# Performance work log

Hardware: AMD Instinct MI355X
Metric: run time of the kernel (lower is better)

Reference implementation:

```python
import jax, jax.numpy as jnp
import numpy as np

# --- model dims (from init args) ---
LAYERS = 6
LEAF = 2 ** (LAYERS - 1)        # 32
M_LEN = 128
CAM_NUM = 2
MAIN_CAM = 0
LATENT = 48
H_LAT = 2048                    # LatentNet hidden
H_BR = 512                      # ChooseBranchNet hidden
B = 16384

# Path bits: for leaf i, bit at classifier depth d (root->leaf order) is
# (i >> (LAYERS-2-d)) & 1. This is exactly what the search_table + double
# advanced-indexing gather in the torch code computes (heap tree routing).
_BITS = ((np.arange(LEAF)[:, None] >> np.arange(LAYERS - 2, -1, -1)[None, :]) & 1)  # [LEAF, LAYERS-1]
BITS = jnp.asarray(_BITS, dtype=jnp.int32)


def setup_inputs() -> dict:
    key = jax.random.key(0)
    ks = jax.random.split(key, 9)
    s = lambda fan: 1.0 / np.sqrt(fan)
    return {
        "batch_data": jax.random.normal(ks[0], (B, CAM_NUM, M_LEN), dtype=jnp.float32),
        # LatentNet: [B, 2*M_LEN] -> hidden -> LEAF*LATENT
        "Wl1": jax.random.normal(ks[1], (2 * M_LEN, H_LAT), dtype=jnp.float32) * s(2 * M_LEN),
        "bl1": jnp.zeros((H_LAT,), dtype=jnp.float32),
        "Wl2": jax.random.normal(ks[2], (H_LAT, LEAF * LATENT), dtype=jnp.float32) * s(H_LAT),
        "bl2": jnp.zeros((LEAF * LATENT,), dtype=jnp.float32),
        # ChooseBranchNet (shared across the LAYERS-1 classifier slots): M_LEN -> hidden -> 2
        "Wb1": jax.random.normal(ks[3], (M_LEN, H_BR), dtype=jnp.float32) * s(M_LEN),
        "bb1": jnp.zeros((H_BR,), dtype=jnp.float32),
        "Wb2": jax.random.normal(ks[4], (H_BR, 2), dtype=jnp.float32) * s(H_BR),
        "bb2": jnp.zeros((2,), dtype=jnp.float32),
    }


def reference(batch_data, Wl1, bl1, Wl2, bl2, Wb1, bb1, Wb2, bb2):
    bsz = batch_data.shape[0]
    # expand_measurements: main cam repeated (LAYERS-1) times -> [B, LAYERS-1, M_LEN]
    main = batch_data[:, MAIN_CAM]                                  # [B, M_LEN]
    x_br = jnp.broadcast_to(main[:, None, :], (bsz, LAYERS - 1, M_LEN))
    # ChooseBranchNet -> per-layer 2-way probabilities
    h = jax.nn.relu(jnp.einsum('blm,mh->blh', x_br, Wb1) + bb1)
    p = jax.nn.softmax(jnp.einsum('blh,ho->blo', h, Wb2) + bb2, axis=-1)  # [B, L-1, 2]
    # Tree gates: product of path-branch probabilities along root->leaf path.
    comp = jnp.where(BITS[None] == 1, p[:, None, :, 1], p[:, None, :, 0])  # [B, LEAF, L-1]
    gates = jnp.prod(comp, axis=-1)                                        # [B, LEAF]
    # top-1 routing (argsort(...)[:, -1] as in the torch code)
    router = jnp.argsort(gates, axis=-1)[:, -1]                            # [B]
    # LatentNet on concatenated two-camera measurements
    x2 = jnp.concatenate([batch_data[:, 0], batch_data[:, 1]], axis=-1)    # [B, 2*M_LEN]
    hl = jax.nn.relu(x2 @ Wl1 + bl1)
    nn_latent = (hl @ Wl2 + bl2).reshape(bsz, LEAF, LATENT)
    # scatter-select per-sample leaf latent (replaces the torch.where loop)
    select = jnp.take_along_axis(nn_latent, router[:, None, None], axis=1)[:, 0]  # [B, LATENT]
    return select
```

## Files before the change

### kernel.cpp

```cpp
#include <hip/hip_runtime.h>
#include <stdint.h>

typedef short bf16x8 __attribute__((ext_vector_type(8)));
typedef float f32x4 __attribute__((ext_vector_type(4)));

#define NROWS 16384
#define K1DIM 256
#define N1DIM 2048
#define N2DIM 96
#define MARGIN 0.03f

#define GLD16(g, l) __builtin_amdgcn_global_load_lds( \
    (const __attribute__((address_space(1))) uint32_t*)(g), \
    (__attribute__((address_space(3))) uint32_t*)(l), 16, 0, 0)

__device__ __forceinline__ ushort f2bf(float x) {
  union { float f; uint32_t u; } c; c.f = x;
  uint32_t u = c.u;
  return (ushort)((u + 0x7FFFu + ((u >> 16) & 1u)) >> 16);
}

__global__ __launch_bounds__(256) void k0_convert(
    const float* __restrict__ bd, const float* __restrict__ Wl1,
    const float* __restrict__ Wl2, const float* __restrict__ Wb1,
    ushort* __restrict__ x2bf, ushort* __restrict__ wl1t,
    ushort* __restrict__ w2t, ushort* __restrict__ wb1t) {
  int i = blockIdx.x * 256 + threadIdx.x;
  {
    float4 v = ((const float4*)bd)[i];
    ushort4 o;
    o.x = f2bf(v.x); o.y = f2bf(v.y); o.z = f2bf(v.z); o.w = f2bf(v.w);
    ((ushort4*)x2bf)[i] = o;
  }
  if (i < 2048 * 256) {
    int n = i >> 8, k = i & 255;
    wl1t[i] = f2bf(Wl1[k * 2048 + n]);
  }
  if (i < 96 * 2048) {
    int j = i >> 11, k = i & 2047;
    int col = (j < 48) ? j : (1440 + j);
    w2t[i] = f2bf(Wl2[k * 1536 + col]);
  }
  if (i < 512 * 128) {
    int j = i >> 7, m = i & 127;
    wb1t[i] = f2bf(Wb1[m * 512 + j]);
  }
}

__global__ __launch_bounds__(256) void k1a_score(
    const ushort* __restrict__ x2bf, const ushort* __restrict__ wb1t,
    const float* __restrict__ bb1, const float* __restrict__ Wb2,
    float* __restrict__ part) {
  __shared__ __align__(1024) ushort As[128 * 64];
  __shared__ __align__(1024) ushort Bs[128 * 64];
  const int t = threadIdx.x, ln = t & 63, wv = t >> 6;
  const int m0 = blockIdx.y << 7;
  const int n0 = blockIdx.x << 7;
  const int wm = (wv >> 1) << 6, wn = (wv & 1) << 6;
  const int rsub = ln >> 3, kc8 = ln & 7;
  const int q = ln >> 4, rr = ln & 15;

  f32x4 acc[4][4] = {};

  for (int k0 = 0; k0 < 128; k0 += 64) {
#pragma unroll
    for (int i = 0; i < 4; i++) {
      int inst = (wv << 2) + i;
      int row = (inst << 3) + rsub;
      GLD16(x2bf + (size_t)(m0 + row) * 256 + k0 + (kc8 << 3), As + (inst << 9));
      GLD16(wb1t + (size_t)(n0 + row) * 128 + k0 + (kc8 << 3), Bs + (inst << 9));
    }
    __syncthreads();
#pragma unroll
    for (int kk = 0; kk < 2; kk++) {
      int kb = ((kk << 2) + q) << 3;
      bf16x8 af[4], bfr[4];
#pragma unroll
      for (int mi = 0; mi < 4; mi++)
        af[mi] = *(const bf16x8*)(As + (((wm + (mi << 4) + rr)) << 6) + kb);
#pragma unroll
      for (int ni = 0; ni < 4; ni++)
        bfr[ni] = *(const bf16x8*)(Bs + (((wn + (ni << 4) + rr)) << 6) + kb);
#pragma unroll
      for (int mi = 0; mi < 4; mi++)
#pragma unroll
        for (int ni = 0; ni < 4; ni++)
          acc[mi][ni] = __builtin_amdgcn_mfma_f32_16x16x32_bf16(
              af[mi], bfr[ni], acc[mi][ni], 0, 0, 0);
    }
    __syncthreads();
  }

  float s4[4][4] = {};
#pragma unroll
  for (int ni = 0; ni < 4; ni++) {
    int col = n0 + wn + (ni << 4) + rr;
    float bias = bb1[col];
    float wdv = Wb2[col * 2 + 1] - Wb2[col * 2];
#pragma unroll
    for (int mi = 0; mi < 4; mi++) {
      f32x4 a = acc[mi][ni];
#pragma unroll
      for (int v = 0; v < 4; v++)
        s4[mi][v] += fmaxf(a[v] + bias, 0.f) * wdv;
    }
  }
#pragma unroll
  for (int off = 1; off <= 8; off <<= 1)
#pragma unroll
    for (int mi = 0; mi < 4; mi++)
#pragma unroll
      for (int v = 0; v < 4; v++)
        s4[mi][v] += __shfl_xor(s4[mi][v], off);

  if (rr == 0) {
    float* dst = part + (size_t)(blockIdx.x * 2 + (wv & 1)) * NROWS +
                 m0 + wm + (q << 2);
#pragma unroll
    for (int mi = 0; mi < 4; mi++) {
      float4 v4 = make_float4(s4[mi][0], s4[mi][1], s4[mi][2], s4[mi][3]);
      *(float4*)(dst + (mi << 4)) = v4;
    }
  }
}

__global__ __launch_bounds__(256) void k1b_classify(
    const float* __restrict__ part, const float* __restrict__ bb2,
    int* __restrict__ router, int* __restrict__ list, int* __restrict__ counter) {
  int t = blockIdx.x * 256 + threadIdx.x;
  float s = bb2[1] - bb2[0];
#pragma unroll
  for (int i = 0; i < 8; i++) s += part[i * NROWS + t];
  router[t] = (s >= 0.f) ? 1 : 0;
  if (fabsf(s) < MARGIN) {
    int idx = atomicAdd(counter, 1);
    list[idx] = t;
  }
}

__global__ __launch_bounds__(256) void k1c_recheck(
    const float* __restrict__ bd, const float* __restrict__ Wb1,
    const float* __restrict__ Wb2, const float* __restrict__ bb1,
    const float* __restrict__ bb2, const int* __restrict__ list,
    const int* __restrict__ counter, int* __restrict__ router) {
  const int ln = threadIdx.x & 63;
  const int wid = (blockIdx.x * 256 + threadIdx.x) >> 6;
  const int count = *counter;
  const float c = bb2[1] - bb2[0];

  for (int base = wid * 4; base < count; base += 512 * 4) {
    int rows[4];
#pragma unroll
    for (int r = 0; r < 4; r++) {
      int idx = base + r;
      rows[r] = list[(idx < count) ? idx : base];
    }
    float acc[4][8];
#pragma unroll
    for (int r = 0; r < 4; r++)
#pragma unroll
      for (int u = 0; u < 8; u++) acc[r][u] = 0.f;

    for (int m = 0; m < 128; m++) {
      float w[8];
#pragma unroll
      for (int u = 0; u < 8; u++) w[u] = Wb1[m * 512 + (u << 6) + ln];
#pragma unroll
      for (int r = 0; r < 4; r++) {
        float x = bd[(size_t)rows[r] * 256 + m];
#pragma unroll
        for (int u = 0; u < 8; u++) acc[r][u] = fmaf(x, w[u], acc[r][u]);
      }
    }
    float sc[4];
#pragma unroll
    for (int r = 0; r < 4; r++) {
      float s = 0.f;
#pragma unroll
      for (int u = 0; u < 8; u++) {
        int j = (u << 6) + ln;
        float wd = Wb2[j * 2 + 1] - Wb2[j * 2];
        s += fmaxf(acc[r][u] + bb1[j], 0.f) * wd;
      }
#pragma unroll
      for (int off = 1; off <= 32; off <<= 1) s += __shfl_xor(s, off);
      sc[r] = s + c;
    }
    if (ln == 0) {
#pragma unroll
      for (int r = 0; r < 4; r++)
        if (base + r < count) router[rows[r]] = (sc[r] >= 0.f) ? 1 : 0;
    }
  }
}

__global__ __launch_bounds__(256, 2) void k2_fused(
    const ushort* __restrict__ x2bf, const ushort* __restrict__ wl1t,
    const ushort* __restrict__ w2t, const float* __restrict__ bl1,
    const float* __restrict__ bl2, const int* __restrict__ router,
    float* __restrict__ out) {
  __shared__ __align__(1024) ushort As[64 * 256];
  __shared__ __align__(1024) ushort Hs[64 * 128];
  __shared__ __align__(1024) ushort Wsm[96 * 128];
  const int t = threadIdx.x, ln = t & 63, wv = t >> 6;
  const int ks2 = blockIdx.x;
  const int m0 = blockIdx.y << 6;
  const int q = ln >> 4, rr = ln & 15;
  const int rg = wv & 1, cg = wv >> 1;

  {
    int s = ln & 31, rh = ln >> 5;
#pragma unroll
    for (int i = 0; i < 8; i++) {
      int inst = (wv << 3) + i;
      int r = (inst << 1) + rh;
      GLD16(x2bf + (size_t)(m0 + r) * 256 + ((s ^ (r & 31)) << 3),
            As + (inst << 9));
    }
  }
  __syncthreads();

  f32x4 accP[2][3] = {};

  for (int nc = 0; nc < 4; nc++) {
    const int n0 = (ks2 << 10) + (nc << 8);
    const int nw = n0 + (wv << 6);

    f32x4 acc1[4][4] = {};
#pragma unroll 4
    for (int kk = 0; kk < 8; kk++) {
      bf16x8 bfr[4];
#pragma unroll
      for (int ni = 0; ni < 4; ni++)
        bfr[ni] = *(const bf16x8*)(wl1t + (size_t)(nw + (ni << 4) + rr) * 256 +
                                   (kk << 5) + (q << 3));
      bf16x8 af[4];
#pragma unroll
      for (int mi = 0; mi < 4; mi++) {
        int row = (mi << 4) + rr;
        af[mi] = *(const bf16x8*)(As + (row << 8) +
                                  ((((kk << 2) + q) ^ (row & 31)) << 3));
      }
#pragma unroll
      for (int mi = 0; mi < 4; mi++)
#pragma unroll
        for (int ni = 0; ni < 4; ni++)
          acc1[mi][ni] = __builtin_amdgcn_mfma_f32_16x16x32_bf16(
              af[mi], bfr[ni], acc1[mi][ni], 0, 0, 0);
    }

#pragma unroll 1
    for (int h = 0; h < 2; h++) {
#pragma unroll
      for (int j = 0; j < 6; j++) {
        int inst = wv * 6 + j;
        int r = (inst << 2) + q;
        GLD16(w2t + (size_t)r * 2048 + n0 + (h << 7) + ((rr ^ (r & 15)) << 3),
              Wsm + (inst << 9));
      }
      if ((wv >> 1) == h) {
#pragma unroll
        for (int ni = 0; ni < 4; ni++) {
          int colh = ((wv & 1) << 6) + (ni << 4) + rr;
          float bias = bl1[nw + (ni << 4) + rr];
#pragma unroll
          for (int mi = 0; mi < 4; mi++) {
            f32x4 a = acc1[mi][ni];
#pragma unroll
            for (int v = 0; v < 4; v++) {
              int row = (mi << 4) + (q << 2) + v;
              Hs[(row << 7) + (((colh >> 3) ^ (row & 15)) << 3) + (colh & 7)] =
                  f2bf(fmaxf(a[v] + bias, 0.f));
            }
          }
        }
      }
      __syncthreads();
#pragma unroll
      for (int kk = 0; kk < 4; kk++) {
        int c = (kk << 2) + q;
        bf16x8 ha[2];
#pragma unroll
        for (int a = 0; a < 2; a++) {
          int row = (rg << 5) + (a << 4) + rr;
          ha[a] = *(const bf16x8*)(Hs + (row << 7) + ((c ^ rr) << 3));
        }
#pragma unroll
        for (int ni = 0; ni < 3; ni++) {
          int jr = cg * 48 + (ni << 4) + rr;
          bf16x8 wb = *(const bf16x8*)(Wsm + (jr << 7) + ((c ^ rr) << 3));
#pragma unroll
          for (int a = 0; a < 2; a++)
            accP[a][ni] = __builtin_amdgcn_mfma_f32_16x16x32_bf16(
                ha[a], wb, accP[a][ni], 0, 0, 0);
        }
      }
      __syncthreads();
    }
  }

#pragma unroll
  for (int a = 0; a < 2; a++) {
#pragma unroll
    for (int v = 0; v < 4; v++) {
      int row = m0 + (rg << 5) + (a << 4) + (q << 2) + v;
      int sel = router[row];
      if (sel == cg) {
        float b0 = 0.f, b1 = 0.f, b2 = 0.f;
        if (ks2 == 0) {
          int bb = sel ? 1488 : 0;
          b0 = bl2[bb + rr];
          b1 = bl2[bb + 16 + rr];
          b2 = bl2[bb + 32 + rr];
        }
        float* ob = out + (size_t)row * 48 + rr;
        atomicAdd(ob, accP[a][0][v] + b0);
        atomicAdd(ob + 16, accP[a][1][v] + b1);
        atomicAdd(ob + 32, accP[a][2][v] + b2);
      }
    }
  }
}

extern "C" void kernel_launch(void* const* d_in, const int* in_sizes, int n_in,
                              void* d_out, int out_size, void* d_ws, size_t ws_size,
                              hipStream_t stream) {
  const float* bd  = (const float*)d_in[0];
  const float* Wl1 = (const float*)d_in[1];
  const float* bl1 = (const float*)d_in[2];
  const float* Wl2 = (const float*)d_in[3];
  const float* bl2 = (const float*)d_in[4];
  const float* Wb1 = (const float*)d_in[5];
  const float* bb1 = (const float*)d_in[6];
  const float* Wb2 = (const float*)d_in[7];
  const float* bb2 = (const float*)d_in[8];

  char* ws = (char*)d_ws;
  ushort* x2bf  = (ushort*)(ws);
  ushort* wl1t  = (ushort*)(ws + 8388608);
  ushort* w2t   = (ushort*)(ws + 9437184);
  int*    router= (int*)(ws + 89522176);
  ushort* wb1t  = (ushort*)(ws + 89587712);
  float*  part  = (float*)(ws + 89718784);
  int*    list  = (int*)(ws + 90243072);
  int*    counter=(int*)(ws + 90308608);
  float*  outp  = (float*)d_out;

  k0_convert<<<dim3(4096), dim3(256), 0, stream>>>(bd, Wl1, Wl2, Wb1,
                                                   x2bf, wl1t, w2t, wb1t);
  hipMemsetAsync(counter, 0, 4, stream);
  hipMemsetAsync(outp, 0, (size_t)out_size * 4, stream);
  k1a_score<<<dim3(4, 128), dim3(256), 0, stream>>>(x2bf, wb1t, bb1, Wb2, part);
  k1b_classify<<<dim3(64), dim3(256), 0, stream>>>(part, bb2, router, list, counter);
  k1c_recheck<<<dim3(128), dim3(256), 0, stream>>>(bd, Wb1, Wb2, bb1, bb2,
                                                   list, counter, router);
  k2_fused<<<dim3(2, 256), dim3(256), 0, stream>>>(x2bf, wl1t, w2t, bl1, bl2,
                                                   router, outp);
}
```

Measured before the change: 183.2 us.

## Bucket rows by router choice so second GEMM computes only selected leaf

Adds a row-map kernel that partitions samples into two contiguous buckets by router value, so each 64-row tile of the fused kernel needs only one 48-column slice of the second-layer weights. This halves the second GEMM's work and weight traffic. The first GEMM is restructured to stage both activations (gathered through the row map) and weight tiles into LDS in K-chunks, with a smaller LDS footprint that allows 3 blocks per CU. The cost is an extra launch, atomics for the bucketing, gathered row loads, and a padding tile in the grid.

```diff
diff --git a/kernel.cpp b/kernel.cpp
--- a/kernel.cpp
+++ b/kernel.cpp
@@ -5,9 +5,9 @@
 typedef float f32x4 __attribute__((ext_vector_type(4)));
 
 #define NROWS 16384
+#define NSLOTS 16448
 #define K1DIM 256
 #define N1DIM 2048
-#define N2DIM 96
 #define MARGIN 0.03f
 
 #define GLD16(g, l) __builtin_amdgcn_global_load_lds( \
@@ -126,14 +126,14 @@
 
 __global__ __launch_bounds__(256) void k1b_classify(
     const float* __restrict__ part, const float* __restrict__ bb2,
-    int* __restrict__ router, int* __restrict__ list, int* __restrict__ counter) {
+    int* __restrict__ router, int* __restrict__ list, int* __restrict__ counters) {
   int t = blockIdx.x * 256 + threadIdx.x;
   float s = bb2[1] - bb2[0];
 #pragma unroll
   for (int i = 0; i < 8; i++) s += part[i * NROWS + t];
   router[t] = (s >= 0.f) ? 1 : 0;
   if (fabsf(s) < MARGIN) {
-    int idx = atomicAdd(counter, 1);
+    int idx = atomicAdd(&counters[0], 1);
     list[idx] = t;
   }
 }
@@ -142,10 +142,10 @@
     const float* __restrict__ bd, const float* __restrict__ Wb1,
     const float* __restrict__ Wb2, const float* __restrict__ bb1,
     const float* __restrict__ bb2, const int* __restrict__ list,
-    const int* __restrict__ counter, int* __restrict__ router) {
+    const int* __restrict__ counters, int* __restrict__ router) {
   const int ln = threadIdx.x & 63;
   const int wid = (blockIdx.x * 256 + threadIdx.x) >> 6;
-  const int count = *counter;
+  const int count = counters[0];
   const float c = bb2[1] - bb2[0];
 
   for (int base = wid * 4; base < count; base += 512 * 4) {
@@ -194,129 +194,152 @@
   }
 }
 
-__global__ __launch_bounds__(256, 2) void k2_fused(
+__global__ __launch_bounds__(256) void k1d_rowmap(
+    const int* __restrict__ router, int* __restrict__ rowmap,
+    int* __restrict__ counters) {
+  int t = blockIdx.x * 256 + threadIdx.x;
+  int sel = router[t];
+  int slot = sel ? (NSLOTS - 1 - atomicAdd(&counters[2], 1))
+                 : atomicAdd(&counters[1], 1);
+  rowmap[slot] = t;
+}
+
+__global__ __launch_bounds__(256, 3) void k2_fused(
     const ushort* __restrict__ x2bf, const ushort* __restrict__ wl1t,
     const ushort* __restrict__ w2t, const float* __restrict__ bl1,
-    const float* __restrict__ bl2, const int* __restrict__ router,
-    float* __restrict__ out) {
-  __shared__ __align__(1024) ushort As[64 * 256];
-  __shared__ __align__(1024) ushort Hs[64 * 128];
-  __shared__ __align__(1024) ushort Wsm[96 * 128];
+    const float* __restrict__ bl2, const int* __restrict__ rowmap,
+    const int* __restrict__ counters, float* __restrict__ out) {
+  __shared__ __align__(1024) ushort As[4096];
+  __shared__ __align__(1024) ushort WtHs[16384];
+  __shared__ __align__(1024) ushort Ws[6144];
+  ushort* Wt = WtHs;
+  ushort* Hs = WtHs;
   const int t = threadIdx.x, ln = t & 63, wv = t >> 6;
   const int ks2 = blockIdx.x;
   const int m0 = blockIdx.y << 6;
   const int q = ln >> 4, rr = ln & 15;
-  const int rg = wv & 1, cg = wv >> 1;
-
-  {
-    int s = ln & 31, rh = ln >> 5;
-#pragma unroll
-    for (int i = 0; i < 8; i++) {
-      int inst = (wv << 3) + i;
-      int r = (inst << 1) + rh;
-      GLD16(x2bf + (size_t)(m0 + r) * 256 + ((s ^ (r & 31)) << 3),
-            As + (inst << 9));
-    }
-  }
-  __syncthreads();
-
-  f32x4 accP[2][3] = {};
+  const int r8 = ln >> 3, s8 = ln & 7;
+  const int r4 = ln >> 4, s16 = ln & 15;
+  const int c0 = counters[1];
+  const int sel_blk = (m0 >= c0) ? 1 : 0;
+  const int selbase = sel_blk * 48;
+
+  int g_as[2];
+#pragma unroll
+  for (int ii = 0; ii < 2; ii++) {
+    int g = rowmap[m0 + (((wv << 1) + ii) << 3) + r8];
+    g_as[ii] = (g < 0) ? 0 : g;
+  }
+
+  f32x4 accP[3] = {};
 
   for (int nc = 0; nc < 4; nc++) {
     const int n0 = (ks2 << 10) + (nc << 8);
-    const int nw = n0 + (wv << 6);
 
     f32x4 acc1[4][4] = {};
-#pragma unroll 4
-    for (int kk = 0; kk < 8; kk++) {
-      bf16x8 bfr[4];
-#pragma unroll
-      for (int ni = 0; ni < 4; ni++)
-        bfr[ni] = *(const bf16x8*)(wl1t + (size_t)(nw + (ni << 4) + rr) * 256 +
-                                   (kk << 5) + (q << 3));
-      bf16x8 af[4];
-#pragma unroll
-      for (int mi = 0; mi < 4; mi++) {
-        int row = (mi << 4) + rr;
-        af[mi] = *(const bf16x8*)(As + (row << 8) +
-                                  ((((kk << 2) + q) ^ (row & 31)) << 3));
-      }
-#pragma unroll
-      for (int mi = 0; mi < 4; mi++)
+#pragma unroll 1
+    for (int ks = 0; ks < 4; ks++) {
+      const int kg = ks << 6;
+#pragma unroll
+      for (int ii = 0; ii < 2; ii++)
+        GLD16(x2bf + (size_t)g_as[ii] * 256 + kg + ((s8 ^ r8) << 3),
+              As + ((((wv << 1) + ii)) << 9));
+#pragma unroll
+      for (int ii = 0; ii < 8; ii++) {
+        int inst = (wv << 3) + ii;
+        int r = (inst << 3) + r8;
+        GLD16(wl1t + (size_t)(n0 + r) * 256 + kg + ((s8 ^ r8) << 3),
+              Wt + (inst << 9));
+      }
+      __syncthreads();
+#pragma unroll
+      for (int kk = 0; kk < 2; kk++) {
+        int c = (kk << 2) + q;
+        int sl = (c ^ (rr & 7)) << 3;
+        bf16x8 af[4], bfv[4];
+#pragma unroll
+        for (int mi = 0; mi < 4; mi++)
+          af[mi] = *(const bf16x8*)(Wt + (((wv << 6) + (mi << 4) + rr) << 6) + sl);
 #pragma unroll
         for (int ni = 0; ni < 4; ni++)
-          acc1[mi][ni] = __builtin_amdgcn_mfma_f32_16x16x32_bf16(
-              af[mi], bfr[ni], acc1[mi][ni], 0, 0, 0);
+          bfv[ni] = *(const bf16x8*)(As + (((ni << 4) + rr) << 6) + sl);
+#pragma unroll
+        for (int mi = 0; mi < 4; mi++)
+#pragma unroll
+          for (int ni = 0; ni < 4; ni++)
+            acc1[mi][ni] = __builtin_amdgcn_mfma_f32_16x16x32_bf16(
+                af[mi], bfv[ni], acc1[mi][ni], 0, 0, 0);
+      }
+      __syncthreads();
+    }
+
+#pragma unroll
+    for (int mi = 0; mi < 4; mi++) {
+      int p = (wv << 4) + (mi << 2) + q;
+      float bias0 = bl1[n0 + (p << 2) + 0];
+      float bias1 = bl1[n0 + (p << 2) + 1];
+      float bias2 = bl1[n0 + (p << 2) + 2];
+      float bias3 = bl1[n0 + (p << 2) + 3];
+#pragma unroll
+      for (int ni = 0; ni < 4; ni++) {
+        int hsrow = (ni << 4) + rr;
+        f32x4 a = acc1[mi][ni];
+        ushort4 pk;
+        pk.x = f2bf(fmaxf(a[0] + bias0, 0.f));
+        pk.y = f2bf(fmaxf(a[1] + bias1, 0.f));
+        pk.z = f2bf(fmaxf(a[2] + bias2, 0.f));
+        pk.w = f2bf(fmaxf(a[3] + bias3, 0.f));
+        *(ushort4*)(Hs + (hsrow << 8) + ((p ^ rr) << 2)) = pk;
+      }
     }
 
 #pragma unroll 1
     for (int h = 0; h < 2; h++) {
 #pragma unroll
-      for (int j = 0; j < 6; j++) {
-        int inst = wv * 6 + j;
-        int r = (inst << 2) + q;
-        GLD16(w2t + (size_t)r * 2048 + n0 + (h << 7) + ((rr ^ (r & 15)) << 3),
-              Wsm + (inst << 9));
-      }
-      if ((wv >> 1) == h) {
-#pragma unroll
-        for (int ni = 0; ni < 4; ni++) {
-          int colh = ((wv & 1) << 6) + (ni << 4) + rr;
-          float bias = bl1[nw + (ni << 4) + rr];
-#pragma unroll
-          for (int mi = 0; mi < 4; mi++) {
-            f32x4 a = acc1[mi][ni];
-#pragma unroll
-            for (int v = 0; v < 4; v++) {
-              int row = (mi << 4) + (q << 2) + v;
-              Hs[(row << 7) + (((colh >> 3) ^ (row & 15)) << 3) + (colh & 7)] =
-                  f2bf(fmaxf(a[v] + bias, 0.f));
-            }
-          }
+      for (int jj = 0; jj < 3; jj++) {
+        int inst = wv * 3 + jj;
+        int r = (inst << 2) + r4;
+        int c = s16 ^ (r & 15);
+        GLD16(w2t + (size_t)(selbase + r) * 2048 + n0 + (h << 7) + (c << 3),
+              Ws + (inst << 9));
+      }
+      __syncthreads();
+#pragma unroll
+      for (int kk = 0; kk < 4; kk++) {
+        int p0 = (h << 5) + (kk << 3) + (q << 1);
+        int hrow = (wv << 4) + rr;
+        union { ushort4 u[2]; bf16x8 v; } hu;
+        hu.u[0] = *(const ushort4*)(Hs + (hrow << 8) + ((p0 ^ rr) << 2));
+        hu.u[1] = *(const ushort4*)(Hs + (hrow << 8) + (((p0 + 1) ^ rr) << 2));
+        int c = (kk << 2) + q;
+#pragma unroll
+        for (int ni = 0; ni < 3; ni++) {
+          bf16x8 wb = *(const bf16x8*)(Ws + (((ni << 4) + rr) << 7) +
+                                       ((c ^ rr) << 3));
+          accP[ni] = __builtin_amdgcn_mfma_f32_16x16x32_bf16(
+              hu.v, wb, accP[ni], 0, 0, 0);
         }
       }
       __syncthreads();
-#pragma unroll
-      for (int kk = 0; kk < 4; kk++) {
-        int c = (kk << 2) + q;
-        bf16x8 ha[2];
-#pragma unroll
-        for (int a = 0; a < 2; a++) {
-          int row = (rg << 5) + (a << 4) + rr;
-          ha[a] = *(const bf16x8*)(Hs + (row << 7) + ((c ^ rr) << 3));
-        }
-#pragma unroll
-        for (int ni = 0; ni < 3; ni++) {
-          int jr = cg * 48 + (ni << 4) + rr;
-          bf16x8 wb = *(const bf16x8*)(Wsm + (jr << 7) + ((c ^ rr) << 3));
-#pragma unroll
-          for (int a = 0; a < 2; a++)
-            accP[a][ni] = __builtin_amdgcn_mfma_f32_16x16x32_bf16(
-                ha[a], wb, accP[a][ni], 0, 0, 0);
-        }
-      }
-      __syncthreads();
-    }
-  }
-
-#pragma unroll
-  for (int a = 0; a < 2; a++) {
+    }
+  }
+
+  {
+    float b[3] = {0.f, 0.f, 0.f};
+    if (ks2 == 0) {
+#pragma unroll
+      for (int ni = 0; ni < 3; ni++)
+        b[ni] = bl2[sel_blk * 1488 + (ni << 4) + rr];
+    }
 #pragma unroll
     for (int v = 0; v < 4; v++) {
-      int row = m0 + (rg << 5) + (a << 4) + (q << 2) + v;
-      int sel = router[row];
-      if (sel == cg) {
-        float b0 = 0.f, b1 = 0.f, b2 = 0.f;
-        if (ks2 == 0) {
-          int bb = sel ? 1488 : 0;
-          b0 = bl2[bb + rr];
-          b1 = bl2[bb + 16 + rr];
-          b2 = bl2[bb + 32 + rr];
-        }
-        float* ob = out + (size_t)row * 48 + rr;
-        atomicAdd(ob, accP[a][0][v] + b0);
-        atomicAdd(ob + 16, accP[a][1][v] + b1);
-        atomicAdd(ob + 32, accP[a][2][v] + b2);
+      int slot = m0 + (wv << 4) + (q << 2) + v;
+      int orig = rowmap[slot];
+      if (orig >= 0) {
+        float* ob = out + (size_t)orig * 48 + rr;
+        atomicAdd(ob, accP[0][v] + b[0]);
+        atomicAdd(ob + 16, accP[1][v] + b[1]);
+        atomicAdd(ob + 32, accP[2][v] + b[2]);
       }
     }
   }
@@ -343,17 +366,21 @@
   ushort* wb1t  = (ushort*)(ws + 89587712);
   float*  part  = (float*)(ws + 89718784);
   int*    list  = (int*)(ws + 90243072);
-  int*    counter=(int*)(ws + 90308608);
+  int*    counters=(int*)(ws + 90308608);
+  int*    rowmap= (int*)(ws + 90310656);
   float*  outp  = (float*)d_out;
 
   k0_convert<<<dim3(4096), dim3(256), 0, stream>>>(bd, Wl1, Wl2, Wb1,
                                                    x2bf, wl1t, w2t, wb1t);
-  hipMemsetAsync(counter, 0, 4, stream);
+  hipMemsetAsync(counters, 0, 12, stream);
+  hipMemsetAsync(rowmap, 0xFF, NSLOTS * 4, stream);
   hipMemsetAsync(outp, 0, (size_t)out_size * 4, stream);
   k1a_score<<<dim3(4, 128), dim3(256), 0, stream>>>(x2bf, wb1t, bb1, Wb2, part);
-  k1b_classify<<<dim3(64), dim3(256), 0, stream>>>(part, bb2, router, list, counter);
+  k1b_classify<<<dim3(64), dim3(256), 0, stream>>>(part, bb2, router, list,
+                                                   counters);
   k1c_recheck<<<dim3(128), dim3(256), 0, stream>>>(bd, Wb1, Wb2, bb1, bb2,
-                                                   list, counter, router);
-  k2_fused<<<dim3(2, 256), dim3(256), 0, stream>>>(x2bf, wl1t, w2t, bl1, bl2,
-                                                   router, outp);
-}
+                                                   list, counters, router);
+  k1d_rowmap<<<dim3(64), dim3(256), 0, stream>>>(router, rowmap, counters);
+  k2_fused<<<dim3(2, 257), dim3(256), 0, stream>>>(x2bf, wl1t, w2t, bl1, bl2,
+                                                   rowmap, counters, outp);
+}
```

Result: no change. 180.0 us (-1.7%).
